# Kernel optimization log

Measured on AMD Instinct MI355X. Metric: run time of the kernel, lower is better.

## Reference

```python
import jax, jax.numpy as jnp
import numpy as np
import math

B, S, E, H = 4, 1024, 1024, 16
HD = E // H
MAX_SEQ = 5000
THETA = 10000.0


def _freqs_cis():
    # RotaryPositionalEncoding buffer: complex64 [MAX_SEQ, E//2]
    freqs = 1.0 / (THETA ** (np.arange(0, E, 2)[: E // 2] / E))
    ang = np.outer(np.arange(MAX_SEQ), freqs)
    return jnp.asarray(np.exp(1j * ang).astype(np.complex64))


def _rope(x, idx, fc_table):
    # x: [B, S, E]; pairs consecutive channels across the FULL embed_dim
    # (applied before head splitting, faithful to the original module)
    xc = x.reshape(*x.shape[:-1], -1, 2)
    xc = jax.lax.complex(xc[..., 0], xc[..., 1])  # [B, S, E//2]
    out = xc * fc_table[idx]                       # [B, S, E//2]
    return jnp.stack([jnp.real(out), jnp.imag(out)], axis=-1).reshape(x.shape)


def reference(query, key, value, query_index, key_index, attn_mask,
              key_padding_mask, Wq, bq, Wk, bk, Wv, bv, Wo, bo):
    q = query @ Wq.T + bq
    k = key @ Wk.T + bk
    v = value @ Wv.T + bv

    fc = _freqs_cis()
    q = _rope(q, query_index, fc)
    k = _rope(k, key_index, fc)

    # torch: q = cat(q.chunk(H, dim=-1), dim=0) -> flat HEAD-MAJOR [H*B, S, HD]
    qf = q.reshape(B, S, H, HD).transpose(2, 0, 1, 3).reshape(H * B, S, HD)
    kf = k.reshape(B, S, H, HD).transpose(2, 0, 1, 3).reshape(H * B, S, HD)
    vf = v.reshape(B, S, H, HD).transpose(2, 0, 1, 3).reshape(H * B, S, HD)

    # mask: logical_or(attn_mask[Sq,Sk], kpm[B,1,Sk]) -> [B, Sq, Sk]
    m = jnp.logical_or(attn_mask[None, :, :], key_padding_mask[:, None, :])
    madd = jnp.where(m, -jnp.inf, 0.0).astype(query.dtype)
    # torch repeat_interleave(H, dim=0) yields BATCH-MAJOR flat [B*H, Sq, Sk];
    # it is added to the head-major scores as-is (faithful to the original
    # indexing, including its head/batch-order quirk)
    madd_flat = jnp.repeat(madd, H, axis=0)

    scores = jnp.einsum('nqd,nkd->nqk', qf / math.sqrt(HD), kf) + madd_flat
    w = jax.nn.softmax(scores, axis=-1)              # [H*B, Sq, Sk]
    of = jnp.einsum('nqk,nkd->nqd', w, vf)           # [H*B, Sq, HD]

    # cat(chunks(dim=0), dim=-1) -> [B, Sq, E], head-major last dim
    attn_output = of.reshape(H, B, S, HD).transpose(1, 2, 0, 3).reshape(B, S, E)
    attn_output = attn_output @ Wo.T + bo

    # stack(chunks(dim=0), dim=1).mean(1) -> [B, Sq, Sk]
    attn_weights = w.reshape(H, B, S, S).transpose(1, 0, 2, 3).mean(axis=1)
    return attn_output, attn_weights


def setup_inputs() -> dict:
    key0 = jax.random.key(0)
    ks = jax.random.split(key0, 10)
    sc = 0.02
    inp = {
        'query': jax.random.normal(ks[0], (B, S, E), jnp.float32),
        'key': jax.random.normal(ks[1], (B, S, E), jnp.float32),
        'value': jax.random.normal(ks[2], (B, S, E), jnp.float32),
        'query_index': jnp.sort(jax.random.randint(ks[3], (B, S), 0, 4096), axis=-1),
        'key_index': jnp.sort(jax.random.randint(ks[4], (B, S), 0, 4096), axis=-1),
        'attn_mask': jnp.triu(jnp.ones((S, S), jnp.bool_), k=1),  # causal
        'key_padding_mask': jnp.zeros((B, S), jnp.bool_),
        'Wq': jax.random.normal(ks[5], (E, E), jnp.float32) * sc,
        'bq': jnp.zeros((E,), jnp.float32),
        'Wk': jax.random.normal(ks[6], (E, E), jnp.float32) * sc,
        'bk': jnp.zeros((E,), jnp.float32),
        'Wv': jax.random.normal(ks[7], (E, E), jnp.float32) * sc,
        'bv': jnp.zeros((E,), jnp.float32),
        'Wo': jax.random.normal(ks[8], (E, E), jnp.float32) * sc,
        'bo': jnp.zeros((E,), jnp.float32),
    }
    return inp
```

## Files before the change

### kernel.cpp

```cpp
#include <hip/hip_runtime.h>
#include <stdint.h>
#include <math.h>

#define B_ 4
#define S_ 1024
#define E_ 1024
#define H_ 16
#define HD_ 64
#define HB_ 64

typedef __attribute__((ext_vector_type(8))) short bhalf8;
typedef __attribute__((ext_vector_type(4))) float floatx4;

__device__ __forceinline__ unsigned short f2bf(float f) {
  union { float f; unsigned u; } v; v.f = f;
  unsigned r = (v.u + 0x7FFFu + ((v.u >> 16) & 1u)) >> 16;
  return (unsigned short)r;
}
__device__ __forceinline__ float bf2f(unsigned short b) {
  union { unsigned u; float f; } v; v.u = ((unsigned)b) << 16;
  return v.f;
}
__device__ __forceinline__ unsigned short f2h(float f) {
  union { _Float16 h; unsigned short u; } v; v.h = (_Float16)f; return v.u;
}
__device__ __forceinline__ float h2f(unsigned short u) {
  union { unsigned short u; _Float16 h; } v; v.u = u; return (float)v.h;
}

__device__ __forceinline__ void gload16(const void* g, void* l) {
  __builtin_amdgcn_global_load_lds(
      (const __attribute__((address_space(1))) unsigned int*)g,
      (__attribute__((address_space(3))) unsigned int*)l, 16, 0, 0);
}

template <int NCH>
__device__ __forceinline__ void stage_tile(const unsigned short* org,
                                           unsigned short* lds, int wave, int lane) {
  const int rl = lane >> 3;
  const int scb = ((lane & 7) << 4) ^ (rl << 4);
  const char* base = (const char*)org + scb;
#pragma unroll
  for (int i = 0; i < NCH / 4; ++i) {
    const int c = wave + 4 * i;
    gload16(base + (size_t)(c * 8 + rl) * 2048, (char*)lds + c * 1024);
  }
}

__device__ __forceinline__ bhalf8 read_frag(const unsigned short* lds, int row, int kbyte) {
  const int off = row * 128 + (kbyte ^ ((row & 7) << 4));
  return *(const bhalf8*)((const char*)lds + off);
}

__global__ void detect_bool_kernel(const uint8_t* __restrict__ amask, int* __restrict__ flag) {
  if (threadIdx.x == 0 && blockIdx.x == 0) *flag = (amask[1] != 0) ? 1 : 0;
}

__global__ __launch_bounds__(256) void cvt_in_kernel(
    const float* __restrict__ q, const float* __restrict__ k,
    const float* __restrict__ v, unsigned short* __restrict__ Ab) {
  const int z = blockIdx.z;
  const float* src = (z == 0) ? q : (z == 1) ? k : v;
  unsigned short* dst = Ab + (size_t)z * 4194304;
  const size_t i = ((size_t)blockIdx.x * 256 + threadIdx.x) * 8;
  float4 a = *(const float4*)(src + i);
  float4 b = *(const float4*)(src + i + 4);
  bhalf8 r;
  r[0] = (short)f2bf(a.x); r[1] = (short)f2bf(a.y);
  r[2] = (short)f2bf(a.z); r[3] = (short)f2bf(a.w);
  r[4] = (short)f2bf(b.x); r[5] = (short)f2bf(b.y);
  r[6] = (short)f2bf(b.z); r[7] = (short)f2bf(b.w);
  *(bhalf8*)(dst + i) = r;
}

__global__ __launch_bounds__(256) void cvt_w_kernel(
    const float* __restrict__ wq, const float* __restrict__ wk,
    const float* __restrict__ wv, const float* __restrict__ wo,
    unsigned short* __restrict__ Wb) {
  const int z = blockIdx.z;
  const float* src = (z == 0) ? wq : (z == 1) ? wk : (z == 2) ? wv : wo;
  unsigned short* dst = Wb + (size_t)z * 1048576;
  const size_t i = ((size_t)blockIdx.x * 256 + threadIdx.x) * 8;
  float4 a = *(const float4*)(src + i);
  float4 b = *(const float4*)(src + i + 4);
  bhalf8 r;
  r[0] = (short)f2bf(a.x); r[1] = (short)f2bf(a.y);
  r[2] = (short)f2bf(a.z); r[3] = (short)f2bf(a.w);
  r[4] = (short)f2bf(b.x); r[5] = (short)f2bf(b.y);
  r[6] = (short)f2bf(b.z); r[7] = (short)f2bf(b.w);
  *(bhalf8*)(dst + i) = r;
}

template <bool BF16OUT>
__global__ __launch_bounds__(256) void mfma_gemm_kernel(
    const unsigned short* __restrict__ A0, const unsigned short* __restrict__ A1,
    const unsigned short* __restrict__ A2,
    const unsigned short* __restrict__ W0, const unsigned short* __restrict__ W1,
    const unsigned short* __restrict__ W2,
    const float* __restrict__ b0, const float* __restrict__ b1,
    const float* __restrict__ b2,
    void* __restrict__ C0, void* __restrict__ C1, void* __restrict__ C2) {
  const int z = blockIdx.z;
  const unsigned short* A = (z == 0) ? A0 : (z == 1) ? A1 : A2;
  const unsigned short* W = (z == 0) ? W0 : (z == 1) ? W1 : W2;
  const float* bias = (z == 0) ? b0 : (z == 1) ? b1 : b2;
  void* C = (z == 0) ? C0 : (z == 1) ? C1 : C2;
  const int lin = blockIdx.y * 8 + blockIdx.x;
  const int swz = (lin & 7) * 32 + (lin >> 3);
  const int m0 = (swz >> 3) * 128, n0 = (swz & 7) * 128;
  __shared__ unsigned short As[128 * 64];
  __shared__ unsigned short Ws[128 * 64];
  const int t = threadIdx.x, wave = t >> 6, lane = t & 63;
  const int wr = wave >> 1, wc = wave & 1;
  floatx4 acc[4][4];
  const floatx4 z4 = {0.f, 0.f, 0.f, 0.f};
#pragma unroll
  for (int i = 0; i < 4; ++i)
#pragma unroll
    for (int j = 0; j < 4; ++j) acc[i][j] = z4;

  for (int k0 = 0; k0 < 1024; k0 += 64) {
    stage_tile<16>(A + (size_t)m0 * 1024 + k0, As, wave, lane);
    stage_tile<16>(W + (size_t)n0 * 1024 + k0, Ws, wave, lane);
    __syncthreads();
#pragma unroll
    for (int ks = 0; ks < 2; ++ks) {
      const int kb = ks * 64 + ((lane >> 4) << 4);
      bhalf8 af[4], bf[4];
#pragma unroll
      for (int mi = 0; mi < 4; ++mi)
        af[mi] = read_frag(As, wr * 64 + mi * 16 + (lane & 15), kb);
#pragma unroll
      for (int ni = 0; ni < 4; ++ni)
        bf[ni] = read_frag(Ws, wc * 64 + ni * 16 + (lane & 15), kb);
#pragma unroll
      for (int mi = 0; mi < 4; ++mi)
#pragma unroll
        for (int ni = 0; ni < 4; ++ni)
          acc[mi][ni] = __builtin_amdgcn_mfma_f32_16x16x32_bf16(af[mi], bf[ni], acc[mi][ni], 0, 0, 0);
    }
    __syncthreads();
  }
#pragma unroll
  for (int mi = 0; mi < 4; ++mi)
#pragma unroll
    for (int ni = 0; ni < 4; ++ni) {
      const int col = n0 + wc * 64 + ni * 16 + (lane & 15);
      const float bv = bias[col];
#pragma unroll
      for (int r = 0; r < 4; ++r) {
        const int row = m0 + wr * 64 + mi * 16 + (lane >> 4) * 4 + r;
        const float v = acc[mi][ni][r] + bv;
        if (BF16OUT)
          ((unsigned short*)C)[(size_t)row * 1024 + col] = f2bf(v);
        else
          ((float*)C)[(size_t)row * 1024 + col] = v;
      }
    }
}

__global__ __launch_bounds__(256) void rope_bf_kernel(unsigned int* __restrict__ X,
                                                      const int* __restrict__ idxs) {
  const int gid = blockIdx.x * 256 + threadIdx.x;
  const int i = gid & 511, bs = gid >> 9;
  const int pos = idxs[bs];
  const double freq = exp(-(double)(2 * i) * (9.210340371976184 / 1024.0));
  const double ang = fmod((double)pos * freq, 6.283185307179586476925287);
  const float fa = (float)ang;
  float sn, c;
  sincosf(fa, &sn, &c);
  const unsigned v = X[gid];
  const float x = bf2f((unsigned short)(v & 0xffffu));
  const float y = bf2f((unsigned short)(v >> 16));
  const float rx = x * c - y * sn;
  const float ry = x * sn + y * c;
  X[gid] = (unsigned)f2bf(rx) | ((unsigned)f2bf(ry) << 16);
}

__global__ __launch_bounds__(256) void transpose_v_kernel(
    const unsigned short* __restrict__ Vr, unsigned short* __restrict__ Vt) {
  const int s0 = blockIdx.x * 64;
  const int bh = blockIdx.y;
  const int b = bh >> 4, h = bh & 15;
  __shared__ unsigned short L[64][72];
  const int t = threadIdx.x, r = t >> 2, cq = (t & 3) * 16;
  const unsigned short* src = Vr + ((size_t)(b * S_) + s0 + r) * E_ + h * HD_ + cq;
  *(bhalf8*)&L[r][cq] = *(const bhalf8*)src;
  *(bhalf8*)&L[r][cq + 8] = *(const bhalf8*)(src + 8);
  __syncthreads();
  bhalf8 o0, o1;
#pragma unroll
  for (int u = 0; u < 8; ++u) o0[u] = (short)L[cq + u][r];
#pragma unroll
  for (int u = 0; u < 8; ++u) o1[u] = (short)L[cq + 8 + u][r];
  unsigned short* dst = Vt + ((size_t)bh * 64 + r) * 1024 + s0 + cq;
  *(bhalf8*)dst = o0;
  *(bhalf8*)(dst + 8) = o1;
}

__global__ __launch_bounds__(256) void fused_sm_kernel(
    const unsigned short* __restrict__ Qr, const unsigned short* __restrict__ Kr,
    unsigned short* __restrict__ P, const void* __restrict__ amask,
    const void* __restrict__ kpm, const int* __restrict__ flagp, int hb0) {
  const int lhb = blockIdx.y, hb = hb0 + lhb;
  const int h = hb >> 2, b = hb & 3, bp = hb >> 4;
  const int q0 = blockIdx.x * 32;
  __shared__ unsigned short Sbuf[32 * 1024];
  const int t = threadIdx.x, w = t >> 6, lane = t & 63;
  const int l4 = lane >> 4, l15 = lane & 15;

  const char* Qbase = (const char*)(Qr + ((size_t)b << 20)) + h * 128;
  const char* Kbase = (const char*)(Kr + ((size_t)b << 20)) + h * 128;

  bhalf8 aq[2][2];
#pragma unroll
  for (int qt = 0; qt < 2; ++qt)
#pragma unroll
    for (int ks = 0; ks < 2; ++ks)
      aq[qt][ks] = *(const bhalf8*)(Qbase + (size_t)(q0 + qt * 16 + l15) * 2048 +
                                    ks * 64 + l4 * 16);

  floatx4 acc[2][16];
  const floatx4 z4 = {0.f, 0.f, 0.f, 0.f};
#pragma unroll
  for (int qt = 0; qt < 2; ++qt)
#pragma unroll
    for (int kt = 0; kt < 16; ++kt) acc[qt][kt] = z4;

  const int kcol0 = w * 256;
#pragma unroll
  for (int kt = 0; kt < 16; ++kt) {
    const char* kb = Kbase + (size_t)(kcol0 + kt * 16 + l15) * 2048 + l4 * 16;
    bhalf8 b0 = *(const bhalf8*)kb;
    bhalf8 b1 = *(const bhalf8*)(kb + 64);
    acc[0][kt] = __builtin_amdgcn_mfma_f32_16x16x32_bf16(aq[0][0], b0, acc[0][kt], 0, 0, 0);
    acc[1][kt] = __builtin_amdgcn_mfma_f32_16x16x32_bf16(aq[1][0], b0, acc[1][kt], 0, 0, 0);
    acc[0][kt] = __builtin_amdgcn_mfma_f32_16x16x32_bf16(aq[0][1], b1, acc[0][kt], 0, 0, 0);
    acc[1][kt] = __builtin_amdgcn_mfma_f32_16x16x32_bf16(aq[1][1], b1, acc[1][kt], 0, 0, 0);
  }

#pragma unroll
  for (int qt = 0; qt < 2; ++qt)
#pragma unroll
    for (int kt = 0; kt < 16; ++kt) {
      const int k = kcol0 + kt * 16 + l15;
#pragma unroll
      for (int r = 0; r < 4; ++r) {
        const int q = qt * 16 + l4 * 4 + r;
        const int off = q * 2048 + ((k * 2) ^ ((q & 7) << 4));
        *(unsigned short*)((char*)Sbuf + off) = f2h(acc[qt][kt][r] * 0.125f);
      }
    }
  __syncthreads();

  const int isu8 = *flagp;
  bool km[16];
  if (isu8) {
    const uint8_t* kp = (const uint8_t*)kpm + (size_t)bp * 1024;
#pragma unroll
    for (int j = 0; j < 4; ++j) {
      uchar4 v = *(const uchar4*)(kp + j * 256 + lane * 4);
      km[j * 4 + 0] = v.x != 0; km[j * 4 + 1] = v.y != 0;
      km[j * 4 + 2] = v.z != 0; km[j * 4 + 3] = v.w != 0;
    }
  } else {
    const int* kp = (const int*)kpm + (size_t)bp * 1024;
#pragma unroll
    for (int j = 0; j < 4; ++j) {
      int4 v = *(const int4*)(kp + j * 256 + lane * 4);
      km[j * 4 + 0] = v.x != 0; km[j * 4 + 1] = v.y != 0;
      km[j * 4 + 2] = v.z != 0; km[j * 4 + 3] = v.w != 0;
    }
  }

  for (int rr = 0; rr < 8; ++rr) {
    const int q = w * 8 + rr;
    const int gq = q0 + q;
    const int xorv = (q & 7) << 4;
    float x[16];
#pragma unroll
    for (int j = 0; j < 4; ++j) {
      const int off = q * 2048 + ((j * 512 + lane * 8) ^ xorv);
      ushort4 hv = *(const ushort4*)((const char*)Sbuf + off);
      x[j * 4 + 0] = h2f(hv.x); x[j * 4 + 1] = h2f(hv.y);
      x[j * 4 + 2] = h2f(hv.z); x[j * 4 + 3] = h2f(hv.w);
    }
    if (isu8) {
      const uint8_t* ap = (const uint8_t*)amask + (size_t)gq * 1024;
#pragma unroll
      for (int j = 0; j < 4; ++j) {
        uchar4 v = *(const uchar4*)(ap + j * 256 + lane * 4);
        if (v.x | km[j * 4 + 0]) x[j * 4 + 0] = -INFINITY;
        if (v.y | km[j * 4 + 1]) x[j * 4 + 1] = -INFINITY;
        if (v.z | km[j * 4 + 2]) x[j * 4 + 2] = -INFINITY;
        if (v.w | km[j * 4 + 3]) x[j * 4 + 3] = -INFINITY;
      }
    } else {
      const int* ap = (const int*)amask + (size_t)gq * 1024;
#pragma unroll
      for (int j = 0; j < 4; ++j) {
        int4 v = *(const int4*)(ap + j * 256 + lane * 4);
        if (v.x || km[j * 4 + 0]) x[j * 4 + 0] = -INFINITY;
        if (v.y || km[j * 4 + 1]) x[j * 4 + 1] = -INFINITY;
        if (v.z || km[j * 4 + 2]) x[j * 4 + 2] = -INFINITY;
        if (v.w || km[j * 4 + 3]) x[j * 4 + 3] = -INFINITY;
      }
    }
    float m = -INFINITY;
#pragma unroll
    for (int i = 0; i < 16; ++i) m = fmaxf(m, x[i]);
    for (int o = 32; o > 0; o >>= 1) m = fmaxf(m, __shfl_xor(m, o));
    float s = 0.f;
#pragma unroll
    for (int i = 0; i < 16; ++i) { x[i] = expf(x[i] - m); s += x[i]; }
    for (int o = 32; o > 0; o >>= 1) s += __shfl_xor(s, o);
    const float inv = 1.0f / s;
    unsigned short* prow = P + ((size_t)lhb << 20) + (size_t)gq * 1024;
#pragma unroll
    for (int j = 0; j < 4; ++j) {
      ushort4 w4;
      w4.x = f2bf(x[j * 4 + 0] * inv); w4.y = f2bf(x[j * 4 + 1] * inv);
      w4.z = f2bf(x[j * 4 + 2] * inv); w4.w = f2bf(x[j * 4 + 3] * inv);
      *(ushort4*)(prow + j * 256 + lane * 4) = w4;
    }
  }
}

__global__ __launch_bounds__(256) void wmean_kernel(
    const unsigned short* __restrict__ P, float* __restrict__ outW,
    int nhh, int first) {
  const size_t gid = (size_t)blockIdx.x * 256 + threadIdx.x;
  const int k8 = (int)(gid & 127);
  const int q = (int)((gid >> 7) & 1023);
  const int b = (int)(gid >> 17);
  float s[8];
#pragma unroll
  for (int u = 0; u < 8; ++u) s[u] = 0.f;
  for (int hh = 0; hh < nhh; ++hh) {
    const int lhb = hh * 4 + b;
    bhalf8 v = *(const bhalf8*)(P + ((size_t)lhb << 20) + ((size_t)q << 10) + k8 * 8);
#pragma unroll
    for (int u = 0; u < 8; ++u) s[u] += bf2f((unsigned short)v[u]);
  }
  float* o = outW + (((size_t)(b * S_ + q)) << 10) + k8 * 8;
  const float invH = 1.0f / 16.0f;
  float4 v0, v1;
  v0.x = s[0] * invH; v0.y = s[1] * invH; v0.z = s[2] * invH; v0.w = s[3] * invH;
  v1.x = s[4] * invH; v1.y = s[5] * invH; v1.z = s[6] * invH; v1.w = s[7] * invH;
  if (!first) {
    float4 a = *(float4*)o, b4 = *(float4*)(o + 4);
    v0.x += a.x; v0.y += a.y; v0.z += a.z; v0.w += a.w;
    v1.x += b4.x; v1.y += b4.y; v1.z += b4.z; v1.w += b4.w;
  }
  *(float4*)o = v0;
  *(float4*)(o + 4) = v1;
}

__global__ __launch_bounds__(256) void pv_mfma_kernel(
    const unsigned short* __restrict__ Wt, const unsigned short* __restrict__ Vt,
    unsigned short* __restrict__ Ocat, int hb0) {
  const int lhb = blockIdx.y, hb = hb0 + lhb;
  const int h = hb >> 2, b = hb & 3;
  const int q0 = blockIdx.x * 64;
  __shared__ unsigned short Ps[64 * 64];
  __shared__ unsigned short Vs[64 * 64];
  const int t = threadIdx.x, wave = t >> 6, lane = t & 63;
  const int wr = wave >> 1, wc = wave & 1;
  const unsigned short* Wh = Wt + ((size_t)lhb << 20);
  const unsigned short* Vh = Vt + (size_t)(b * 16 + h) * 65536;
  floatx4 acc[2][2];
  const floatx4 z4 = {0.f, 0.f, 0.f, 0.f};
#pragma unroll
  for (int i = 0; i < 2; ++i)
#pragma unroll
    for (int j = 0; j < 2; ++j) acc[i][j] = z4;

  for (int k0 = 0; k0 < 1024; k0 += 64) {
    stage_tile<8>(Wh + (size_t)q0 * 1024 + k0, Ps, wave, lane);
    stage_tile<8>(Vh + k0, Vs, wave, lane);
    __syncthreads();
#pragma unroll
    for (int ks = 0; ks < 2; ++ks) {
      const int kb = ks * 64 + ((lane >> 4) << 4);
      bhalf8 af[2], bf[2];
#pragma unroll
      for (int mi = 0; mi < 2; ++mi)
        af[mi] = read_frag(Ps, wr * 32 + mi * 16 + (lane & 15), kb);
#pragma unroll
      for (int ni = 0; ni < 2; ++ni)
        bf[ni] = read_frag(Vs, wc * 32 + ni * 16 + (lane & 15), kb);
#pragma unroll
      for (int mi = 0; mi < 2; ++mi)
#pragma unroll
        for (int ni = 0; ni < 2; ++ni)
          acc[mi][ni] = __builtin_amdgcn_mfma_f32_16x16x32_bf16(af[mi], bf[ni], acc[mi][ni], 0, 0, 0);
    }
    __syncthreads();
  }
#pragma unroll
  for (int mi = 0; mi < 2; ++mi)
#pragma unroll
    for (int ni = 0; ni < 2; ++ni) {
      const int d = wc * 32 + ni * 16 + (lane & 15);
#pragma unroll
      for (int r = 0; r < 4; ++r) {
        const int q = q0 + wr * 32 + mi * 16 + (lane >> 4) * 4 + r;
        Ocat[((size_t)(b * S_) + q) * E_ + h * HD_ + d] = f2bf(acc[mi][ni][r]);
      }
    }
}

extern "C" void kernel_launch(void* const* d_in, const int* in_sizes, int n_in,
                              void* d_out, int out_size, void* d_ws, size_t ws_size,
                              hipStream_t stream) {
  (void)in_sizes; (void)n_in; (void)out_size;
  const float* query = (const float*)d_in[0];
  const float* key   = (const float*)d_in[1];
  const float* value = (const float*)d_in[2];
  const int* qidx = (const int*)d_in[3];
  const int* kidx = (const int*)d_in[4];
  const void* amask = d_in[5];
  const void* kpm   = d_in[6];
  const float* Wq = (const float*)d_in[7];
  const float* bq = (const float*)d_in[8];
  const float* Wk = (const float*)d_in[9];
  const float* bk = (const float*)d_in[10];
  const float* Wv = (const float*)d_in[11];
  const float* bv = (const float*)d_in[12];
  const float* Wo = (const float*)d_in[13];
  const float* bo = (const float*)d_in[14];

  float* outA = (float*)d_out;
  float* outW = (float*)d_out + (size_t)B_ * S_ * E_;

  float* ws = (float*)d_ws;
  unsigned short* Ab   = (unsigned short*)(ws + 0);
  unsigned short* Wb   = (unsigned short*)(ws + 6291456);
  unsigned short* Qr   = (unsigned short*)(ws + 8388608);
  unsigned short* Kr   = (unsigned short*)(ws + 10485760);
  unsigned short* Vr   = (unsigned short*)(ws + 12582912);
  unsigned short* Vt   = (unsigned short*)(ws + 14680064);
  unsigned short* Ocat = (unsigned short*)(ws + 16777216);
  int* flagp           = (int*)(ws + 18874368);
  const size_t tail_off = 18874432;

  const size_t ws_floats = ws_size / 4;
  int CH = 0;
  unsigned short* P = nullptr;
  for (int c = 64; c >= 4; c >>= 1) {
    if (tail_off + (size_t)c * 524288 <= ws_floats) {
      CH = c;
      P = (unsigned short*)(ws + tail_off);
      break;
    }
  }
  if (!CH) {
    CH = 8;
    P = (unsigned short*)ws;
  }

  detect_bool_kernel<<<1, 64, 0, stream>>>((const uint8_t*)amask, flagp);

  cvt_in_kernel<<<dim3(2048, 1, 3), 256, 0, stream>>>(query, key, value, Ab);
  cvt_w_kernel<<<dim3(512, 1, 4), 256, 0, stream>>>(Wq, Wk, Wv, Wo, Wb);

  mfma_gemm_kernel<true><<<dim3(8, 32, 3), 256, 0, stream>>>(
      Ab, Ab + 4194304, Ab + 8388608,
      Wb, Wb + 1048576, Wb + 2097152,
      bq, bk, bv, Qr, Kr, Vr);

  rope_bf_kernel<<<8192, 256, 0, stream>>>((unsigned int*)Qr, qidx);
  rope_bf_kernel<<<8192, 256, 0, stream>>>((unsigned int*)Kr, kidx);

  transpose_v_kernel<<<dim3(16, 64), 256, 0, stream>>>(Vr, Vt);

  const int nch = HB_ / CH;
  for (int c = 0; c < nch; ++c) {
    const int hb0 = c * CH;
    fused_sm_kernel<<<dim3(32, CH), 256, 0, stream>>>(Qr, Kr, P, amask, kpm,
                                                      flagp, hb0);
    wmean_kernel<<<2048, 256, 0, stream>>>(P, outW, CH / 4, (c == 0) ? 1 : 0);
    pv_mfma_kernel<<<dim3(16, CH), 256, 0, stream>>>(P, Vt, Ocat, hb0);
  }

  mfma_gemm_kernel<false><<<dim3(8, 32, 1), 256, 0, stream>>>(
      Ocat, Ocat, Ocat, Wb + 3145728, Wb + 3145728, Wb + 3145728,
      bo, bo, bo, outA, outA, outA);
}
```

Baseline: 271.3 us.

## Halve softmax query tile, transpose MFMA operands, vectorize LDS/mask/P accesses, use exp2

The fused QK-softmax kernel now handles 16 query rows per block instead of 32, which halves shared memory and accumulator registers and doubles the grid. K becomes the A operand so each lane holds four consecutive keys and can write them to LDS as one ushort4 instead of scalar stores. Mask, LDS and P accesses move from 4-wide to 8-wide vectors, and the scale is folded into an exp2 FMA. The cost is that each K tile is now loaded by twice as many blocks, so K reuse per block drops.

After: 255.5 us. 1.06x faster.

```diff
diff --git a/kernel.cpp b/kernel.cpp
--- a/kernel.cpp
+++ b/kernel.cpp
@@ -204,53 +204,44 @@
     const void* __restrict__ kpm, const int* __restrict__ flagp, int hb0) {
   const int lhb = blockIdx.y, hb = hb0 + lhb;
   const int h = hb >> 2, b = hb & 3, bp = hb >> 4;
-  const int q0 = blockIdx.x * 32;
-  __shared__ unsigned short Sbuf[32 * 1024];
+  const int q0 = blockIdx.x * 16;
+  __shared__ unsigned short Sbuf[16 * 1024];
   const int t = threadIdx.x, w = t >> 6, lane = t & 63;
   const int l4 = lane >> 4, l15 = lane & 15;
 
   const char* Qbase = (const char*)(Qr + ((size_t)b << 20)) + h * 128;
   const char* Kbase = (const char*)(Kr + ((size_t)b << 20)) + h * 128;
 
-  bhalf8 aq[2][2];
-#pragma unroll
-  for (int qt = 0; qt < 2; ++qt)
-#pragma unroll
-    for (int ks = 0; ks < 2; ++ks)
-      aq[qt][ks] = *(const bhalf8*)(Qbase + (size_t)(q0 + qt * 16 + l15) * 2048 +
-                                    ks * 64 + l4 * 16);
-
-  floatx4 acc[2][16];
+  bhalf8 bq0 = *(const bhalf8*)(Qbase + (size_t)(q0 + l15) * 2048 + l4 * 16);
+  bhalf8 bq1 = *(const bhalf8*)(Qbase + (size_t)(q0 + l15) * 2048 + 64 + l4 * 16);
+
+  floatx4 acc[16];
   const floatx4 z4 = {0.f, 0.f, 0.f, 0.f};
 #pragma unroll
-  for (int qt = 0; qt < 2; ++qt)
-#pragma unroll
-    for (int kt = 0; kt < 16; ++kt) acc[qt][kt] = z4;
-
-  const int kcol0 = w * 256;
-#pragma unroll
-  for (int kt = 0; kt < 16; ++kt) {
-    const char* kb = Kbase + (size_t)(kcol0 + kt * 16 + l15) * 2048 + l4 * 16;
-    bhalf8 b0 = *(const bhalf8*)kb;
-    bhalf8 b1 = *(const bhalf8*)(kb + 64);
-    acc[0][kt] = __builtin_amdgcn_mfma_f32_16x16x32_bf16(aq[0][0], b0, acc[0][kt], 0, 0, 0);
-    acc[1][kt] = __builtin_amdgcn_mfma_f32_16x16x32_bf16(aq[1][0], b0, acc[1][kt], 0, 0, 0);
-    acc[0][kt] = __builtin_amdgcn_mfma_f32_16x16x32_bf16(aq[0][1], b1, acc[0][kt], 0, 0, 0);
-    acc[1][kt] = __builtin_amdgcn_mfma_f32_16x16x32_bf16(aq[1][1], b1, acc[1][kt], 0, 0, 0);
-  }
-
-#pragma unroll
-  for (int qt = 0; qt < 2; ++qt)
-#pragma unroll
-    for (int kt = 0; kt < 16; ++kt) {
-      const int k = kcol0 + kt * 16 + l15;
-#pragma unroll
-      for (int r = 0; r < 4; ++r) {
-        const int q = qt * 16 + l4 * 4 + r;
-        const int off = q * 2048 + ((k * 2) ^ ((q & 7) << 4));
-        *(unsigned short*)((char*)Sbuf + off) = f2h(acc[qt][kt][r] * 0.125f);
-      }
-    }
+  for (int i = 0; i < 16; ++i) acc[i] = z4;
+
+  const int krow0 = w * 256;
+#pragma unroll
+  for (int mt = 0; mt < 16; ++mt) {
+    const char* kr = Kbase + (size_t)(krow0 + mt * 16 + l15) * 2048 + l4 * 16;
+    bhalf8 a0 = *(const bhalf8*)kr;
+    bhalf8 a1 = *(const bhalf8*)(kr + 64);
+    acc[mt] = __builtin_amdgcn_mfma_f32_16x16x32_bf16(a0, bq0, acc[mt], 0, 0, 0);
+    acc[mt] = __builtin_amdgcn_mfma_f32_16x16x32_bf16(a1, bq1, acc[mt], 0, 0, 0);
+  }
+
+  {
+    const int q = l15;
+    const int xorv = (q & 7) << 4;
+#pragma unroll
+    for (int mt = 0; mt < 16; ++mt) {
+      const int kb2 = (krow0 + mt * 16 + l4 * 4) * 2;
+      ushort4 hv;
+      hv.x = f2h(acc[mt][0]); hv.y = f2h(acc[mt][1]);
+      hv.z = f2h(acc[mt][2]); hv.w = f2h(acc[mt][3]);
+      *(ushort4*)((char*)Sbuf + q * 2048 + (kb2 ^ xorv)) = hv;
+    }
+  }
   __syncthreads();
 
   const int isu8 = *flagp;
@@ -258,70 +249,89 @@
   if (isu8) {
     const uint8_t* kp = (const uint8_t*)kpm + (size_t)bp * 1024;
 #pragma unroll
-    for (int j = 0; j < 4; ++j) {
-      uchar4 v = *(const uchar4*)(kp + j * 256 + lane * 4);
-      km[j * 4 + 0] = v.x != 0; km[j * 4 + 1] = v.y != 0;
-      km[j * 4 + 2] = v.z != 0; km[j * 4 + 3] = v.w != 0;
+    for (int j = 0; j < 2; ++j) {
+      uint2 mv = *(const uint2*)(kp + j * 512 + lane * 8);
+#pragma unroll
+      for (int u = 0; u < 4; ++u) {
+        km[j * 8 + u] = ((mv.x >> (8 * u)) & 0xffu) != 0;
+        km[j * 8 + 4 + u] = ((mv.y >> (8 * u)) & 0xffu) != 0;
+      }
     }
   } else {
     const int* kp = (const int*)kpm + (size_t)bp * 1024;
 #pragma unroll
-    for (int j = 0; j < 4; ++j) {
-      int4 v = *(const int4*)(kp + j * 256 + lane * 4);
-      km[j * 4 + 0] = v.x != 0; km[j * 4 + 1] = v.y != 0;
-      km[j * 4 + 2] = v.z != 0; km[j * 4 + 3] = v.w != 0;
-    }
-  }
-
-  for (int rr = 0; rr < 8; ++rr) {
-    const int q = w * 8 + rr;
-    const int gq = q0 + q;
-    const int xorv = (q & 7) << 4;
+    for (int j = 0; j < 2; ++j) {
+      int4 v0 = *(const int4*)(kp + j * 512 + lane * 8);
+      int4 v1 = *(const int4*)(kp + j * 512 + lane * 8 + 4);
+      km[j * 8 + 0] = v0.x != 0; km[j * 8 + 1] = v0.y != 0;
+      km[j * 8 + 2] = v0.z != 0; km[j * 8 + 3] = v0.w != 0;
+      km[j * 8 + 4] = v1.x != 0; km[j * 8 + 5] = v1.y != 0;
+      km[j * 8 + 6] = v1.z != 0; km[j * 8 + 7] = v1.w != 0;
+    }
+  }
+
+  const float C = 0.18033688011112042f;
+  for (int rr = 0; rr < 4; ++rr) {
+    const int ql = w * 4 + rr;
+    const int gq = q0 + ql;
+    const int xr = (ql & 7) << 4;
     float x[16];
 #pragma unroll
-    for (int j = 0; j < 4; ++j) {
-      const int off = q * 2048 + ((j * 512 + lane * 8) ^ xorv);
-      ushort4 hv = *(const ushort4*)((const char*)Sbuf + off);
-      x[j * 4 + 0] = h2f(hv.x); x[j * 4 + 1] = h2f(hv.y);
-      x[j * 4 + 2] = h2f(hv.z); x[j * 4 + 3] = h2f(hv.w);
+    for (int j = 0; j < 2; ++j) {
+      const int off = ql * 2048 + ((j * 1024 + lane * 16) ^ xr);
+      bhalf8 hv = *(const bhalf8*)((const char*)Sbuf + off);
+#pragma unroll
+      for (int u = 0; u < 8; ++u) x[j * 8 + u] = h2f((unsigned short)hv[u]);
     }
     if (isu8) {
       const uint8_t* ap = (const uint8_t*)amask + (size_t)gq * 1024;
 #pragma unroll
-      for (int j = 0; j < 4; ++j) {
-        uchar4 v = *(const uchar4*)(ap + j * 256 + lane * 4);
-        if (v.x | km[j * 4 + 0]) x[j * 4 + 0] = -INFINITY;
-        if (v.y | km[j * 4 + 1]) x[j * 4 + 1] = -INFINITY;
-        if (v.z | km[j * 4 + 2]) x[j * 4 + 2] = -INFINITY;
-        if (v.w | km[j * 4 + 3]) x[j * 4 + 3] = -INFINITY;
+      for (int j = 0; j < 2; ++j) {
+        uint2 mv = *(const uint2*)(ap + j * 512 + lane * 8);
+#pragma unroll
+        for (int u = 0; u < 4; ++u) {
+          if (((mv.x >> (8 * u)) & 0xffu) || km[j * 8 + u]) x[j * 8 + u] = -INFINITY;
+          if (((mv.y >> (8 * u)) & 0xffu) || km[j * 8 + 4 + u]) x[j * 8 + 4 + u] = -INFINITY;
+        }
       }
     } else {
       const int* ap = (const int*)amask + (size_t)gq * 1024;
 #pragma unroll
-      for (int j = 0; j < 4; ++j) {
-        int4 v = *(const int4*)(ap + j * 256 + lane * 4);
-        if (v.x || km[j * 4 + 0]) x[j * 4 + 0] = -INFINITY;
-        if (v.y || km[j * 4 + 1]) x[j * 4 + 1] = -INFINITY;
-        if (v.z || km[j * 4 + 2]) x[j * 4 + 2] = -INFINITY;
-        if (v.w || km[j * 4 + 3]) x[j * 4 + 3] = -INFINITY;
+      for (int j = 0; j < 2; ++j) {
+        int4 v0 = *(const int4*)(ap + j * 512 + lane * 8);
+        int4 v1 = *(const int4*)(ap + j * 512 + lane * 8 + 4);
+        if (v0.x || km[j * 8 + 0]) x[j * 8 + 0] = -INFINITY;
+        if (v0.y || km[j * 8 + 1]) x[j * 8 + 1] = -INFINITY;
+        if (v0.z || km[j * 8 + 2]) x[j * 8 + 2] = -INFINITY;
+        if (v0.w || km[j * 8 + 3]) x[j * 8 + 3] = -INFINITY;
+        if (v1.x || km[j * 8 + 4]) x[j * 8 + 4] = -INFINITY;
+        if (v1.y || km[j * 8 + 5]) x[j * 8 + 5] = -INFINITY;
+        if (v1.z || km[j * 8 + 6]) x[j * 8 + 6] = -INFINITY;
+        if (v1.w || km[j * 8 + 7]) x[j * 8 + 7] = -INFINITY;
       }
     }
-    float m = -INFINITY;
-#pragma unroll
-    for (int i = 0; i < 16; ++i) m = fmaxf(m, x[i]);
+    float m = x[0];
+#pragma unroll
+    for (int i = 1; i < 16; ++i) m = fmaxf(m, x[i]);
+#pragma unroll
     for (int o = 32; o > 0; o >>= 1) m = fmaxf(m, __shfl_xor(m, o));
+    const float mc = m * C;
     float s = 0.f;
 #pragma unroll
-    for (int i = 0; i < 16; ++i) { x[i] = expf(x[i] - m); s += x[i]; }
+    for (int i = 0; i < 16; ++i) {
+      x[i] = exp2f(__builtin_fmaf(x[i], C, -mc));
+      s += x[i];
+    }
+#pragma unroll
     for (int o = 32; o > 0; o >>= 1) s += __shfl_xor(s, o);
     const float inv = 1.0f / s;
-    unsigned short* prow = P + ((size_t)lhb << 20) + (size_t)gq * 1024;
-#pragma unroll
-    for (int j = 0; j < 4; ++j) {
-      ushort4 w4;
-      w4.x = f2bf(x[j * 4 + 0] * inv); w4.y = f2bf(x[j * 4 + 1] * inv);
-      w4.z = f2bf(x[j * 4 + 2] * inv); w4.w = f2bf(x[j * 4 + 3] * inv);
-      *(ushort4*)(prow + j * 256 + lane * 4) = w4;
+    unsigned short* prow = P + ((size_t)lhb << 20) + ((size_t)gq << 10);
+#pragma unroll
+    for (int j = 0; j < 2; ++j) {
+      bhalf8 pv;
+#pragma unroll
+      for (int u = 0; u < 8; ++u) pv[u] = (short)f2bf(x[j * 8 + u] * inv);
+      *(bhalf8*)(prow + j * 512 + lane * 8) = pv;
     }
   }
 }
@@ -477,7 +487,7 @@
   const int nch = HB_ / CH;
   for (int c = 0; c < nch; ++c) {
     const int hb0 = c * CH;
-    fused_sm_kernel<<<dim3(32, CH), 256, 0, stream>>>(Qr, Kr, P, amask, kpm,
+    fused_sm_kernel<<<dim3(64, CH), 256, 0, stream>>>(Qr, Kr, P, amask, kpm,
                                                       flagp, hb0);
     wmean_kernel<<<2048, 256, 0, stream>>>(P, outW, CH / 4, (c == 0) ? 1 : 0);
     pv_mfma_kernel<<<dim3(16, CH), 256, 0, stream>>>(P, Vt, Ocat, hb0);
```
